# Kernel tuning notes

Hardware: AMD Instinct MI355X
Metric: run time of the kernel (lower is better)

Reference implementation:

```python
import jax, jax.numpy as jnp
import numpy as np

LN_EPS = 1e-5


def setup_inputs() -> dict:
    key = jax.random.key(0)
    kA, kX, kh = jax.random.split(key, 3)
    B, N, Cin, C, K = 16, 1024, 64, 64, 3
    A = jax.random.normal(kA, (B, N, N), dtype=jnp.float32)
    X = jax.random.normal(kX, (B, N, Cin), dtype=jnp.float32)
    h = jax.random.normal(kh, (K + 1, C, N), dtype=jnp.float32)
    ln_gamma = jnp.ones((C,), dtype=jnp.float32)
    ln_beta = jnp.zeros((C,), dtype=jnp.float32)
    return {"A": A, "X": X, "h": h, "ln_gamma": ln_gamma, "ln_beta": ln_beta}


def reference(A, X, h, ln_gamma, ln_beta):
    # Original loops compute, for each output channel c:
    #   sum_i sum_ch diag(h[i,c]) @ A^i @ X[..., ch]
    # which equals sum_i h[i,c,:] * (A^i @ X.sum(-1)).
    num_terms = h.shape[0] - 1  # static
    Xs = X.sum(-1)  # [B, N]
    powers = [Xs]
    p = Xs
    for _ in range(num_terms):  # static small loop over polynomial terms
        p = jnp.einsum('bnm,bm->bn', A, p)  # A^i @ Xs, matrix-vector per batch
        powers.append(p)
    P = jnp.stack(powers)  # [K+1, B, N]
    # node-variant per-channel taps: Y[b,n,c] = sum_i h[i,c,n] * P[i,b,n]
    Y = jnp.einsum('icn,ibn->bnc', h, P)  # [B, N, C]
    mu = Y.mean(axis=-1, keepdims=True)
    var = Y.var(axis=-1, keepdims=True)
    Yn = (Y - mu) / jnp.sqrt(var + LN_EPS) * ln_gamma + ln_beta
    return jnp.tanh(Yn)
```

## Files before the change

kernel.cpp:

```cpp
#include <hip/hip_runtime.h>
#include <math.h>

constexpr int B = 16, N = 1024, Cin = 64, C = 64, K = 3;
constexpr int BN = B * N;
constexpr int GRID = 512;
constexpr int ROWS = 32;
#define LN_EPS 1e-5f

__device__ __forceinline__ void bbar(unsigned int* cnt) {
    __syncthreads();
    if (threadIdx.x == 0) {
        __hip_atomic_fetch_add(cnt, 1u, __ATOMIC_RELAXED, __HIP_MEMORY_SCOPE_AGENT);
        int spins = 0;
        while (__hip_atomic_load(cnt, __ATOMIC_RELAXED, __HIP_MEMORY_SCOPE_AGENT) < 32u) {
            __builtin_amdgcn_s_sleep(8);
            if (++spins > (1 << 17)) break;
        }
    }
    __syncthreads();
}

__device__ __forceinline__ void matvec4(const float* __restrict__ Ab,
                                        const float4* __restrict__ xs,
                                        int row, int lane,
                                        float& a0, float& a1, float& a2, float& a3) {
    const float4* r0 = (const float4*)(Ab + (size_t)(row + 0) * N);
    const float4* r1 = (const float4*)(Ab + (size_t)(row + 1) * N);
    const float4* r2 = (const float4*)(Ab + (size_t)(row + 2) * N);
    const float4* r3 = (const float4*)(Ab + (size_t)(row + 3) * N);
    a0 = a1 = a2 = a3 = 0.f;
    #pragma unroll
    for (int k = 0; k < 4; ++k) {
        int idx = k * 64 + lane;
        float4 xx = xs[idx];
        float4 v0 = r0[idx];
        float4 v1 = r1[idx];
        float4 v2 = r2[idx];
        float4 v3 = r3[idx];
        a0 += v0.x * xx.x + v0.y * xx.y + v0.z * xx.z + v0.w * xx.w;
        a1 += v1.x * xx.x + v1.y * xx.y + v1.z * xx.z + v1.w * xx.w;
        a2 += v2.x * xx.x + v2.y * xx.y + v2.z * xx.z + v2.w * xx.w;
        a3 += v3.x * xx.x + v3.y * xx.y + v3.z * xx.z + v3.w * xx.w;
    }
    #pragma unroll
    for (int off = 32; off; off >>= 1) {
        a0 += __shfl_xor(a0, off);
        a1 += __shfl_xor(a1, off);
        a2 += __shfl_xor(a2, off);
        a3 += __shfl_xor(a3, off);
    }
}

__global__ void __launch_bounds__(256)
fused_persist(const float* __restrict__ A, const float* __restrict__ X,
              const float* __restrict__ h, const float* __restrict__ gamma,
              const float* __restrict__ beta, float* __restrict__ out,
              unsigned int* __restrict__ bar, float* __restrict__ P) {
    __shared__ float hl[K + 1][ROWS][C];
    __shared__ __align__(16) float4 xs[N / 4];
    __shared__ float p3s[ROWS];
    const int tid   = threadIdx.x;
    const int lane  = tid & 63;
    const int w     = tid >> 6;
    const int b     = blockIdx.x >> 5;
    const int rbase = (blockIdx.x & 31) * ROWS;
    unsigned int* mybar = bar + (size_t)b * 3 * 32;

    {
        const float* Xb = X + ((size_t)b * N + rbase) * Cin;
        float* P0 = P + (size_t)b * N;
        #pragma unroll
        for (int j = 0; j < 8; ++j) {
            int nn = w * 8 + j;
            float v = Xb[(size_t)nn * Cin + lane];
            #pragma unroll
            for (int off = 32; off; off >>= 1) v += __shfl_xor(v, off);
            if (lane == 0)
                __hip_atomic_store(&P0[rbase + nn], v, __ATOMIC_RELAXED,
                                   __HIP_MEMORY_SCOPE_AGENT);
        }
    }

    {
        const float* src = h + ((size_t)w * C + lane) * N + rbase;
        #pragma unroll
        for (int j4 = 0; j4 < 8; ++j4) {
            float4 v = ((const float4*)src)[j4];
            hl[w][j4 * 4 + 0][lane] = v.x;
            hl[w][j4 * 4 + 1][lane] = v.y;
            hl[w][j4 * 4 + 2][lane] = v.z;
            hl[w][j4 * 4 + 3][lane] = v.w;
        }
    }
    bbar(mybar);

    const float* Ab = A + ((size_t)b << 20);
    for (int it = 0; it < 3; ++it) {
        const float* xsrc = P + (size_t)it * BN + (size_t)b * N;
        xs[tid] = ((const float4*)xsrc)[tid];
        __syncthreads();
        float* ydst = P + (size_t)(it + 1) * BN + (size_t)b * N;
        #pragma unroll
        for (int r = 0; r < 2; ++r) {
            const int row = rbase + r * 16 + w * 4;
            float a0, a1, a2, a3;
            matvec4(Ab, xs, row, lane, a0, a1, a2, a3);
            if (lane == 0) {
                if (it < 2) {
                    __hip_atomic_store(&ydst[row + 0], a0, __ATOMIC_RELAXED, __HIP_MEMORY_SCOPE_AGENT);
                    __hip_atomic_store(&ydst[row + 1], a1, __ATOMIC_RELAXED, __HIP_MEMORY_SCOPE_AGENT);
                    __hip_atomic_store(&ydst[row + 2], a2, __ATOMIC_RELAXED, __HIP_MEMORY_SCOPE_AGENT);
                    __hip_atomic_store(&ydst[row + 3], a3, __ATOMIC_RELAXED, __HIP_MEMORY_SCOPE_AGENT);
                } else {
                    int o = r * 16 + w * 4;
                    p3s[o + 0] = a0; p3s[o + 1] = a1; p3s[o + 2] = a2; p3s[o + 3] = a3;
                }
            }
        }
        if (it < 2) bbar(mybar + (1 + it) * 32);
        else        __syncthreads();
    }

    const float g  = gamma[lane];
    const float be = beta[lane];
    #pragma unroll
    for (int j = 0; j < 8; ++j) {
        const int nn = w * 8 + j;
        const int n  = rbase + nn;
        float y = p3s[nn] * hl[3][nn][lane];
        #pragma unroll
        for (int i = 0; i < 3; ++i) {
            float pv = P[(size_t)i * BN + (size_t)b * N + n];
            y += pv * hl[i][nn][lane];
        }
        float s = y;
        #pragma unroll
        for (int off = 32; off; off >>= 1) s += __shfl_xor(s, off);
        float mu = s * (1.0f / 64.0f);
        float d  = y - mu;
        float v  = d * d;
        #pragma unroll
        for (int off = 32; off; off >>= 1) v += __shfl_xor(v, off);
        float var = v * (1.0f / 64.0f);
        float yn  = d * rsqrtf(var + LN_EPS) * g + be;
        out[((size_t)b * N + n) * C + lane] = tanhf(yn);
    }
}

extern "C" void kernel_launch(void* const* d_in, const int* in_sizes, int n_in,
                              void* d_out, int out_size, void* d_ws, size_t ws_size,
                              hipStream_t stream) {
    const float* A     = (const float*)d_in[0];
    const float* X     = (const float*)d_in[1];
    const float* h     = (const float*)d_in[2];
    const float* gamma = (const float*)d_in[3];
    const float* beta  = (const float*)d_in[4];
    float* out = (float*)d_out;

    unsigned int* bar = (unsigned int*)d_ws;
    float* P = (float*)((char*)d_ws + 8192);

    hipMemsetAsync(bar, 0, B * 3 * 32 * sizeof(unsigned int), stream);
    fused_persist<<<GRID, 256, 0, stream>>>(A, X, h, gamma, beta, out, bar, P);
}
```

Measured before the change: 121.1 us.

## Keep the block's A rows in registers across all three matvec iterations

Each wave now loads its 8 rows of A (32 float4 per lane) into registers once at kernel start, before the X reduction and the first barrier. All three power iterations reuse these registers. Previously A was re-read from global memory (or L2/MALL) three times. This cuts A traffic from 3x to 1x and lets the A load overlap the setup phase, at the cost of 128 extra VGPRs per thread, which could limit occupancy or cause spills.

```diff
diff --git a/kernel.cpp b/kernel.cpp
--- a/kernel.cpp
+++ b/kernel.cpp
@@ -20,37 +20,6 @@
     __syncthreads();
 }
 
-__device__ __forceinline__ void matvec4(const float* __restrict__ Ab,
-                                        const float4* __restrict__ xs,
-                                        int row, int lane,
-                                        float& a0, float& a1, float& a2, float& a3) {
-    const float4* r0 = (const float4*)(Ab + (size_t)(row + 0) * N);
-    const float4* r1 = (const float4*)(Ab + (size_t)(row + 1) * N);
-    const float4* r2 = (const float4*)(Ab + (size_t)(row + 2) * N);
-    const float4* r3 = (const float4*)(Ab + (size_t)(row + 3) * N);
-    a0 = a1 = a2 = a3 = 0.f;
-    #pragma unroll
-    for (int k = 0; k < 4; ++k) {
-        int idx = k * 64 + lane;
-        float4 xx = xs[idx];
-        float4 v0 = r0[idx];
-        float4 v1 = r1[idx];
-        float4 v2 = r2[idx];
-        float4 v3 = r3[idx];
-        a0 += v0.x * xx.x + v0.y * xx.y + v0.z * xx.z + v0.w * xx.w;
-        a1 += v1.x * xx.x + v1.y * xx.y + v1.z * xx.z + v1.w * xx.w;
-        a2 += v2.x * xx.x + v2.y * xx.y + v2.z * xx.z + v2.w * xx.w;
-        a3 += v3.x * xx.x + v3.y * xx.y + v3.z * xx.z + v3.w * xx.w;
-    }
-    #pragma unroll
-    for (int off = 32; off; off >>= 1) {
-        a0 += __shfl_xor(a0, off);
-        a1 += __shfl_xor(a1, off);
-        a2 += __shfl_xor(a2, off);
-        a3 += __shfl_xor(a3, off);
-    }
-}
-
 __global__ void __launch_bounds__(256)
 fused_persist(const float* __restrict__ A, const float* __restrict__ X,
               const float* __restrict__ h, const float* __restrict__ gamma,
@@ -65,6 +34,18 @@
     const int b     = blockIdx.x >> 5;
     const int rbase = (blockIdx.x & 31) * ROWS;
     unsigned int* mybar = bar + (size_t)b * 3 * 32;
+
+    const float* Ab = A + ((size_t)b << 20);
+    float4 Ar[2][4][4];
+    #pragma unroll
+    for (int r = 0; r < 2; ++r)
+        #pragma unroll
+        for (int j = 0; j < 4; ++j) {
+            const float4* rp = (const float4*)(Ab + (size_t)(rbase + r * 16 + w * 4 + j) * N);
+            #pragma unroll
+            for (int k = 0; k < 4; ++k)
+                Ar[r][j][k] = rp[k * 64 + lane];
+        }
 
     {
         const float* Xb = X + ((size_t)b * N + rbase) * Cin;
@@ -94,27 +75,46 @@
     }
     bbar(mybar);
 
-    const float* Ab = A + ((size_t)b << 20);
     for (int it = 0; it < 3; ++it) {
         const float* xsrc = P + (size_t)it * BN + (size_t)b * N;
         xs[tid] = ((const float4*)xsrc)[tid];
         __syncthreads();
-        float* ydst = P + (size_t)(it + 1) * BN + (size_t)b * N;
+
+        float acc[2][4] = {{0.f, 0.f, 0.f, 0.f}, {0.f, 0.f, 0.f, 0.f}};
         #pragma unroll
-        for (int r = 0; r < 2; ++r) {
-            const int row = rbase + r * 16 + w * 4;
-            float a0, a1, a2, a3;
-            matvec4(Ab, xs, row, lane, a0, a1, a2, a3);
-            if (lane == 0) {
-                if (it < 2) {
-                    __hip_atomic_store(&ydst[row + 0], a0, __ATOMIC_RELAXED, __HIP_MEMORY_SCOPE_AGENT);
-                    __hip_atomic_store(&ydst[row + 1], a1, __ATOMIC_RELAXED, __HIP_MEMORY_SCOPE_AGENT);
-                    __hip_atomic_store(&ydst[row + 2], a2, __ATOMIC_RELAXED, __HIP_MEMORY_SCOPE_AGENT);
-                    __hip_atomic_store(&ydst[row + 3], a3, __ATOMIC_RELAXED, __HIP_MEMORY_SCOPE_AGENT);
-                } else {
-                    int o = r * 16 + w * 4;
-                    p3s[o + 0] = a0; p3s[o + 1] = a1; p3s[o + 2] = a2; p3s[o + 3] = a3;
+        for (int k = 0; k < 4; ++k) {
+            float4 xx = xs[k * 64 + lane];
+            #pragma unroll
+            for (int r = 0; r < 2; ++r)
+                #pragma unroll
+                for (int j = 0; j < 4; ++j) {
+                    float4 a = Ar[r][j][k];
+                    acc[r][j] += a.x * xx.x + a.y * xx.y + a.z * xx.z + a.w * xx.w;
                 }
+        }
+        #pragma unroll
+        for (int off = 32; off; off >>= 1)
+            #pragma unroll
+            for (int r = 0; r < 2; ++r)
+                #pragma unroll
+                for (int j = 0; j < 4; ++j)
+                    acc[r][j] += __shfl_xor(acc[r][j], off);
+
+        if (lane == 0) {
+            if (it < 2) {
+                float* ydst = P + (size_t)(it + 1) * BN + (size_t)b * N;
+                #pragma unroll
+                for (int r = 0; r < 2; ++r)
+                    #pragma unroll
+                    for (int j = 0; j < 4; ++j)
+                        __hip_atomic_store(&ydst[rbase + r * 16 + w * 4 + j], acc[r][j],
+                                           __ATOMIC_RELAXED, __HIP_MEMORY_SCOPE_AGENT);
+            } else {
+                #pragma unroll
+                for (int r = 0; r < 2; ++r)
+                    #pragma unroll
+                    for (int j = 0; j < 4; ++j)
+                        p3s[r * 16 + w * 4 + j] = acc[r][j];
             }
         }
         if (it < 2) bbar(mybar + (1 + it) * 32);
```

Result: no change. 121.9 us (+0.7%).
